# Performance work log

Measured on AMD Instinct MI355X. Metric: run time of the kernel, lower is better.

Reference implementation:

```python
import jax, jax.numpy as jnp
import numpy as np

B, N, E, H, HID = 4, 2048, 1024, 16, 4096
D = E // H
EPS = 1e-5


def setup_inputs() -> dict:
    key = jax.random.key(0)
    ks = jax.random.split(key, 8)
    s = 0.02
    return {
        "x": jax.random.normal(ks[0], (B, N, E), dtype=jnp.float32),
        "Wqkv": jax.random.normal(ks[1], (3 * E, E), dtype=jnp.float32) * s,
        "bqkv": jnp.zeros((3 * E,), dtype=jnp.float32),
        "Wo": jax.random.normal(ks[2], (E, E), dtype=jnp.float32) * s,
        "bo": jnp.zeros((E,), dtype=jnp.float32),
        "ln1_g": jnp.ones((E,), dtype=jnp.float32),
        "ln1_b": jnp.zeros((E,), dtype=jnp.float32),
        "W1": jax.random.normal(ks[3], (HID, E), dtype=jnp.float32) * s,
        "bf1": jnp.zeros((HID,), dtype=jnp.float32),
        "W2": jax.random.normal(ks[4], (E, HID), dtype=jnp.float32) * s,
        "bf2": jnp.zeros((E,), dtype=jnp.float32),
        "ln2_g": jnp.ones((E,), dtype=jnp.float32),
        "ln2_b": jnp.zeros((E,), dtype=jnp.float32),
    }


def _layernorm(x, g, b):
    m = jnp.mean(x, axis=-1, keepdims=True)
    v = jnp.mean(jnp.square(x - m), axis=-1, keepdims=True)
    return (x - m) * jax.lax.rsqrt(v + EPS) * g + b


def reference(x, Wqkv, bqkv, Wo, bo, ln1_g, ln1_b, W1, bf1, W2, bf2, ln2_g, ln2_b):
    Bx, Nx, Ex = x.shape
    # --- MultiHeadSelfAttention (faithful to original, including its einsum-label quirk) ---
    qkv = x @ Wqkv.T + bqkv                                   # (B,N,3E)
    qkv = qkv.reshape(Bx, Nx, 3, H, D).transpose(2, 0, 3, 1, 4)  # (3,B,H,N,D)
    q, k, v = qkv[0], qkv[1], qkv[2]                          # each (B,H,N,D)
    # original torch labels: q/k interpreted as (n,q,h,d) -> energy (B,N,H,H)
    energy = jnp.einsum('nqhd,nkhd->nhqk', q, k)
    attention = jax.nn.softmax(energy / (Ex ** 0.5), axis=-1)  # softmax over heads axis
    out = jnp.einsum('nhql,nlhd->nqhd', attention, v).reshape(Bx, Nx, Ex)
    attn_out = out @ Wo.T + bo
    # --- residual + LN1 ---
    h = _layernorm(x + attn_out, ln1_g, ln1_b)
    # --- FFN (dropout is identity in eval) ---
    f = jax.nn.gelu(h @ W1.T + bf1, approximate=False) @ W2.T + bf2
    # --- residual + LN2 ---
    return _layernorm(h + f, ln2_g, ln2_b)
```

## Files before the change

kernel.cpp:

```cpp
#include <hip/hip_runtime.h>
#include <hip/hip_bf16.h>
#include <math.h>

typedef __hip_bfloat16 bf16;
typedef __bf16 bf8v __attribute__((ext_vector_type(8)));
typedef float f4v __attribute__((ext_vector_type(4)));

__device__ inline void storeC(bf16* p, float v) { *p = __float2bfloat16(v); }
__device__ inline void storeC(float* p, float v) { *p = v; }

__device__ inline void gld16(const void* g, void* l) {
    __builtin_amdgcn_global_load_lds(
        (__attribute__((address_space(1))) void*)g,
        (__attribute__((address_space(3))) void*)l, 16, 0, 0);
}

__global__ __launch_bounds__(256)
void cast_f2b(const float* __restrict__ X, bf16* __restrict__ Y, long n)
{
    const long i = ((long)blockIdx.x * 256 + threadIdx.x) * 4;
    if (i + 3 < n) {
        const float4 v = *(const float4*)(X + i);
        Y[i + 0] = __float2bfloat16(v.x);
        Y[i + 1] = __float2bfloat16(v.y);
        Y[i + 2] = __float2bfloat16(v.z);
        Y[i + 3] = __float2bfloat16(v.w);
    }
}

template<int ACT, bool HASRES, typename CT, int K>
__global__ __launch_bounds__(256)
void gemm_bt(const bf16* __restrict__ A, const bf16* __restrict__ W,
             const float* __restrict__ bias, const float* __restrict__ R,
             CT* __restrict__ C, int M, int N)
{
    __shared__ __align__(16) unsigned short sA[2 * 128 * 32];
    __shared__ __align__(16) unsigned short sB[2 * 128 * 32];

    const int tid  = threadIdx.x;
    const int lane = tid & 63;
    const int wave = tid >> 6;
    const long row0 = (long)blockIdx.x * 128;
    const long col0 = (long)blockIdx.y * 128;
    const int wm = (wave >> 1) * 64;
    const int wn = (wave & 1) * 64;
    const int fr = lane & 15;
    const int fk = (lane >> 4) * 8;

    const f4v fzero = {0.f, 0.f, 0.f, 0.f};
    f4v acc[4][4];
#pragma unroll
    for (int i = 0; i < 4; ++i)
#pragma unroll
        for (int j = 0; j < 4; ++j) acc[i][j] = fzero;

    const unsigned short* gA = (const unsigned short*)A + (row0 + (tid >> 2)) * (long)K + (tid & 3) * 8;
    const unsigned short* gB = (const unsigned short*)W + (col0 + (tid >> 2)) * (long)K + (tid & 3) * 8;
    unsigned short* lA0 = &sA[wave * 512];
    unsigned short* lA1 = &sA[2048 + wave * 512];
    unsigned short* lB0 = &sB[wave * 512];
    unsigned short* lB1 = &sB[2048 + wave * 512];

    gld16(gA,                lA0);
    gld16(gA + 64 * (long)K, lA1);
    gld16(gB,                lB0);
    gld16(gB + 64 * (long)K, lB1);
    __syncthreads();

    constexpr int NI = K >> 5;
#pragma unroll 2
    for (int i = 0; i < NI; ++i) {
        if (i + 1 < NI) {
            const int kn = (i + 1) << 5;
            const int nb = ((i + 1) & 1) * 4096;
            gld16(gA + kn,                lA0 + nb);
            gld16(gA + 64 * (long)K + kn, lA1 + nb);
            gld16(gB + kn,                lB0 + nb);
            gld16(gB + 64 * (long)K + kn, lB1 + nb);
        }

        const int base = (i & 1) * 4096;
        bf8v af[4], bv[4];
#pragma unroll
        for (int t = 0; t < 4; ++t) {
            af[t] = *(const bf8v*)&sA[base + (wm + t * 16 + fr) * 32 + fk];
            bv[t] = *(const bf8v*)&sB[base + (wn + t * 16 + fr) * 32 + fk];
        }
#pragma unroll
        for (int ii = 0; ii < 4; ++ii)
#pragma unroll
            for (int jj = 0; jj < 4; ++jj)
                acc[ii][jj] = __builtin_amdgcn_mfma_f32_16x16x32_bf16(af[ii], bv[jj], acc[ii][jj], 0, 0, 0);

        __syncthreads();
    }

#pragma unroll
    for (int j = 0; j < 4; ++j) {
        const long n = col0 + wn + j * 16 + fr;
        const float bvv = bias[n];
#pragma unroll
        for (int i = 0; i < 4; ++i) {
            const long mbase = row0 + wm + i * 16 + (lane >> 4) * 4;
#pragma unroll
            for (int r = 0; r < 4; ++r) {
                float v0 = acc[i][j][r] + bvv;
                if (HASRES) v0 += R[(mbase + r) * (long)N + n];
                if (ACT == 1) v0 = 0.5f * v0 * (1.f + erff(v0 * 0.70710678118654752f));
                storeC(&C[(mbase + r) * (long)N + n], v0);
            }
        }
    }
}

__global__ __launch_bounds__(256)
void attn_kernel(const bf16* __restrict__ qkv, bf16* __restrict__ scr)
{
    __shared__ float sb[4][3392];
    const int tid = threadIdx.x;
    const int wave = tid >> 6, lane = tid & 63;
    const int m = blockIdx.x * 4 + wave;

    float* q = sb[wave];
    float* k = q + 1040;
    float* v = k + 1040;
    float* a = v + 1040;

    const bf16* rowp = qkv + (size_t)m * 3072;
    for (int i = lane; i < 1024; i += 64) {
        int hh = i >> 6, dd = i & 63;
        q[hh * 65 + dd] = __bfloat162float(rowp[i]);
        k[hh * 65 + dd] = __bfloat162float(rowp[1024 + i]);
        v[hh * 65 + dd] = __bfloat162float(rowp[2048 + i]);
    }
    __syncthreads();

    const int h1 = lane & 15, qd = lane >> 4;
    float e[4];
#pragma unroll
    for (int j = 0; j < 4; ++j) {
        const float* qr = q + h1 * 65;
        const float* kr = k + (qd * 4 + j) * 65;
        float s0 = 0.f;
        for (int d = 0; d < 64; ++d) s0 += qr[d] * kr[d];
        e[j] = s0 * 0.03125f;
    }
    float mx = fmaxf(fmaxf(e[0], e[1]), fmaxf(e[2], e[3]));
    mx = fmaxf(mx, __shfl_xor(mx, 16, 64));
    mx = fmaxf(mx, __shfl_xor(mx, 32, 64));
    float p[4], ps = 0.f;
#pragma unroll
    for (int j = 0; j < 4; ++j) { p[j] = expf(e[j] - mx); ps += p[j]; }
    ps += __shfl_xor(ps, 16, 64);
    ps += __shfl_xor(ps, 32, 64);
    const float inv = 1.f / ps;
#pragma unroll
    for (int j = 0; j < 4; ++j) a[h1 * 17 + qd * 4 + j] = p[j] * inv;
    __syncthreads();

    const int h = lane & 15, dg = lane >> 4;
    float arow[16];
#pragma unroll
    for (int l2 = 0; l2 < 16; ++l2) arow[l2] = a[h * 17 + l2];
    const int b = m >> 11, j = m & 2047;
    bf16* op = scr + (((size_t)b * 2048 + h * 128 + (j >> 4)) * 1024 + (j & 15) * 64);
    for (int t = 0; t < 16; ++t) {
        const int d = dg * 16 + t;
        float o = 0.f;
#pragma unroll
        for (int l2 = 0; l2 < 16; ++l2) o += arow[l2] * v[l2 * 65 + d];
        op[d] = __float2bfloat16(o);
    }
}

__global__ __launch_bounds__(256)
void ln_kernel(const float* __restrict__ X, const float* __restrict__ G,
               const float* __restrict__ Bt, float* __restrict__ Y32,
               bf16* __restrict__ Yb)
{
    __shared__ float rs[4], rq[4];
    const int tid = threadIdx.x;
    const long row = blockIdx.x;
    const float* xp = X + row * 1024;
    float x[4];
#pragma unroll
    for (int i = 0; i < 4; ++i) x[i] = xp[tid + 256 * i];

    float s = x[0] + x[1] + x[2] + x[3];
#pragma unroll
    for (int off = 32; off; off >>= 1) s += __shfl_down(s, off, 64);
    if ((tid & 63) == 0) rs[tid >> 6] = s;
    __syncthreads();
    const float mean = (rs[0] + rs[1] + rs[2] + rs[3]) * (1.f / 1024.f);

    float qv = 0.f;
#pragma unroll
    for (int i = 0; i < 4; ++i) { float d = x[i] - mean; qv += d * d; }
#pragma unroll
    for (int off = 32; off; off >>= 1) qv += __shfl_down(qv, off, 64);
    if ((tid & 63) == 0) rq[tid >> 6] = qv;
    __syncthreads();
    const float var = (rq[0] + rq[1] + rq[2] + rq[3]) * (1.f / 1024.f);
    const float rstd = rsqrtf(var + 1e-5f);

#pragma unroll
    for (int i = 0; i < 4; ++i) {
        const int e = tid + 256 * i;
        const float yv = (x[i] - mean) * rstd * G[e] + Bt[e];
        Y32[row * 1024 + e] = yv;
        if (Yb) Yb[row * 1024 + e] = __float2bfloat16(yv);
    }
}

extern "C" void kernel_launch(void* const* d_in, const int* in_sizes, int n_in,
                              void* d_out, int out_size, void* d_ws, size_t ws_size,
                              hipStream_t stream)
{
    (void)in_sizes; (void)n_in; (void)out_size;
    const float* x    = (const float*)d_in[0];
    const float* Wqkv = (const float*)d_in[1];
    const float* bqkv = (const float*)d_in[2];
    const float* Wo   = (const float*)d_in[3];
    const float* bo   = (const float*)d_in[4];
    const float* g1   = (const float*)d_in[5];
    const float* b1   = (const float*)d_in[6];
    const float* W1   = (const float*)d_in[7];
    const float* bf1  = (const float*)d_in[8];
    const float* W2   = (const float*)d_in[9];
    const float* bf2  = (const float*)d_in[10];
    const float* g2   = (const float*)d_in[11];
    const float* b2   = (const float*)d_in[12];
    float* out = (float*)d_out;

    if (ws_size < 125829120ULL) return;

    char* ws = (char*)d_ws;
    bf16* qkv   = (bf16*)(ws + 0);
    float* t    = (float*)(ws + 0);
    bf16* u     = (bf16*)(ws + 0);
    bf16* Wqkvb = (bf16*)(ws + 67108864);
    bf16* Wob   = (bf16*)(ws + 73400320);
    bf16* W1b   = (bf16*)(ws + 75497472);
    bf16* W2b   = (bf16*)(ws + 83886080);
    bf16* xb    = (bf16*)(ws + 92274688);
    bf16* scr   = (bf16*)(ws + 92274688);
    bf16* hb    = (bf16*)(ws + 109051904);
    float* h    = out;

    cast_f2b<<<8192, 256, 0, stream>>>(x,    xb,    8388608);
    cast_f2b<<<3072, 256, 0, stream>>>(Wqkv, Wqkvb, 3145728);
    cast_f2b<<<1024, 256, 0, stream>>>(Wo,   Wob,   1048576);
    cast_f2b<<<4096, 256, 0, stream>>>(W1,   W1b,   4194304);
    cast_f2b<<<4096, 256, 0, stream>>>(W2,   W2b,   4194304);

    gemm_bt<0, false, bf16, 1024><<<dim3(64, 24), 256, 0, stream>>>(xb, Wqkvb, bqkv, nullptr, qkv, 8192, 3072);
    attn_kernel<<<2048, 256, 0, stream>>>(qkv, scr);
    gemm_bt<0, true, float, 1024><<<dim3(64, 8), 256, 0, stream>>>(scr, Wob, bo, x, t, 8192, 1024);
    ln_kernel<<<8192, 256, 0, stream>>>(t, g1, b1, h, hb);
    gemm_bt<1, false, bf16, 1024><<<dim3(64, 32), 256, 0, stream>>>(hb, W1b, bf1, nullptr, u, 8192, 4096);
    gemm_bt<0, true, float, 4096><<<dim3(64, 8), 256, 0, stream>>>(u, W2b, bf2, h, out, 8192, 1024);
    ln_kernel<<<8192, 256, 0, stream>>>(out, g2, b2, out, nullptr);
}
```

Baseline: 514.9 us.

## Replace 128x128 GEMM with 256-row tiles, 4-stage LDS pipeline and swizzle

Replaces the 128x128 double-buffered bf16 GEMM with a 512-thread kernel that computes 256xBN tiles (BN 256 or 128). It adds a 4-slot LDS ring with explicit vmcnt waits, an XOR swizzle to avoid LDS bank conflicts, an XCD-aware block-id remap, and s_setprio around the MFMA bursts. The aim is more data reuse per block and better overlap of global loads with matrix math. In exchange it uses much more LDS (up to 128 KB dynamic) and more registers, and the grid is smaller, which may limit occupancy and cause wave quantisation on the smaller GEMMs.

```diff
diff --git a/kernel.cpp b/kernel.cpp
--- a/kernel.cpp
+++ b/kernel.cpp
@@ -28,84 +28,110 @@
     }
 }
 
-template<int ACT, bool HASRES, typename CT, int K>
-__global__ __launch_bounds__(256)
-void gemm_bt(const bf16* __restrict__ A, const bf16* __restrict__ W,
-             const float* __restrict__ bias, const float* __restrict__ R,
-             CT* __restrict__ C, int M, int N)
-{
-    __shared__ __align__(16) unsigned short sA[2 * 128 * 32];
-    __shared__ __align__(16) unsigned short sB[2 * 128 * 32];
+template<int ACT, bool HASRES, typename CT, int K, int BN>
+__global__ __launch_bounds__(512, 2)
+void gemm256(const bf16* __restrict__ A, const bf16* __restrict__ W,
+             const float* __restrict__ bias, const float* __restrict__ Rr,
+             CT* __restrict__ C, int N)
+{
+    extern __shared__ __align__(16) unsigned short lds[];
+    constexpr int NT   = K / 32;
+    constexpr int NREP = BN / 64;
+    constexpr int A_SH = 256 * 32;
+    constexpr int SLOT = A_SH + BN * 32;
+
+    int id = blockIdx.y * gridDim.x + blockIdx.x;
+    const int nwg = gridDim.x * gridDim.y;
+    id = (id & 7) * (nwg >> 3) + (id >> 3);
+    const int bm = id % gridDim.x;
+    const int bn = id / gridDim.x;
+    const long row0 = (long)bm * 256;
+    const long col0 = (long)bn * BN;
 
     const int tid  = threadIdx.x;
     const int lane = tid & 63;
     const int wave = tid >> 6;
-    const long row0 = (long)blockIdx.x * 128;
-    const long col0 = (long)blockIdx.y * 128;
-    const int wm = (wave >> 1) * 64;
-    const int wn = (wave & 1) * 64;
+    const int wm = wave >> 2;
+    const int wn = wave & 3;
     const int fr = lane & 15;
-    const int fk = (lane >> 4) * 8;
-
-    const f4v fzero = {0.f, 0.f, 0.f, 0.f};
-    f4v acc[4][4];
-#pragma unroll
-    for (int i = 0; i < 4; ++i)
-#pragma unroll
-        for (int j = 0; j < 4; ++j) acc[i][j] = fzero;
-
-    const unsigned short* gA = (const unsigned short*)A + (row0 + (tid >> 2)) * (long)K + (tid & 3) * 8;
-    const unsigned short* gB = (const unsigned short*)W + (col0 + (tid >> 2)) * (long)K + (tid & 3) * 8;
-    unsigned short* lA0 = &sA[wave * 512];
-    unsigned short* lA1 = &sA[2048 + wave * 512];
-    unsigned short* lB0 = &sB[wave * 512];
-    unsigned short* lB1 = &sB[2048 + wave * 512];
-
-    gld16(gA,                lA0);
-    gld16(gA + 64 * (long)K, lA1);
-    gld16(gB,                lB0);
-    gld16(gB + 64 * (long)K, lB1);
-    __syncthreads();
-
-    constexpr int NI = K >> 5;
-#pragma unroll 2
-    for (int i = 0; i < NI; ++i) {
-        if (i + 1 < NI) {
-            const int kn = (i + 1) << 5;
-            const int nb = ((i + 1) & 1) * 4096;
-            gld16(gA + kn,                lA0 + nb);
-            gld16(gA + 64 * (long)K + kn, lA1 + nb);
-            gld16(gB + kn,                lB0 + nb);
-            gld16(gB + 64 * (long)K + kn, lB1 + nb);
+    const int ksw = (((lane >> 4) ^ ((lane >> 2) & 3)) << 3);
+
+    const int srow = tid >> 2;
+    const int csrc = (tid & 3) ^ ((srow >> 2) & 3);
+    const unsigned short* gA = (const unsigned short*)A + (row0 + srow) * (long)K + csrc * 8;
+    const unsigned short* gB = (const unsigned short*)W + (col0 + srow) * (long)K + csrc * 8;
+    unsigned short* const wbase = lds + wave * 512;
+
+    auto stage = [&](int t) {
+        const long k0 = (long)t * 32;
+        unsigned short* sl = wbase + (t & 3) * SLOT;
+        gld16(gA + k0,                 sl);
+        gld16(gA + 128 * (long)K + k0, sl + 4096);
+        gld16(gB + k0,                 sl + A_SH);
+        if constexpr (BN == 256)
+            gld16(gB + 128 * (long)K + k0, sl + A_SH + 4096);
+    };
+
+    f4v acc[8][NREP];
+#pragma unroll
+    for (int i = 0; i < 8; ++i)
+#pragma unroll
+        for (int j = 0; j < NREP; ++j) acc[i][j] = {0.f, 0.f, 0.f, 0.f};
+
+    stage(0); stage(1); stage(2);
+
+#pragma unroll 4
+    for (int t = 0; t < NT; ++t) {
+        if constexpr (BN == 256) {
+            if (t + 2 < NT)      asm volatile("s_waitcnt vmcnt(8)" ::: "memory");
+            else if (t + 1 < NT) asm volatile("s_waitcnt vmcnt(4)" ::: "memory");
+            else                 asm volatile("s_waitcnt vmcnt(0)" ::: "memory");
+        } else {
+            if (t + 2 < NT)      asm volatile("s_waitcnt vmcnt(6)" ::: "memory");
+            else if (t + 1 < NT) asm volatile("s_waitcnt vmcnt(3)" ::: "memory");
+            else                 asm volatile("s_waitcnt vmcnt(0)" ::: "memory");
         }
-
-        const int base = (i & 1) * 4096;
-        bf8v af[4], bv[4];
-#pragma unroll
-        for (int t = 0; t < 4; ++t) {
-            af[t] = *(const bf8v*)&sA[base + (wm + t * 16 + fr) * 32 + fk];
-            bv[t] = *(const bf8v*)&sB[base + (wn + t * 16 + fr) * 32 + fk];
+        __builtin_amdgcn_s_barrier();
+        __builtin_amdgcn_sched_barrier(0);
+        if (t + 3 < NT) stage(t + 3);
+
+        const unsigned short* sA = lds + (t & 3) * SLOT;
+        const unsigned short* sB = sA + A_SH;
+
+        bf8v bfrag[NREP];
+#pragma unroll
+        for (int ni = 0; ni < NREP; ++ni)
+            bfrag[ni] = *(const bf8v*)&sB[(wn * (NREP * 16) + ni * 16 + fr) * 32 + ksw];
+
+#pragma unroll
+        for (int ph = 0; ph < 2; ++ph) {
+            bf8v afrag[4];
+#pragma unroll
+            for (int mi = 0; mi < 4; ++mi)
+                afrag[mi] = *(const bf8v*)&sA[(wm * 128 + ph * 64 + mi * 16 + fr) * 32 + ksw];
+            __builtin_amdgcn_s_setprio(1);
+#pragma unroll
+            for (int mi = 0; mi < 4; ++mi)
+#pragma unroll
+                for (int ni = 0; ni < NREP; ++ni)
+                    acc[ph * 4 + mi][ni] = __builtin_amdgcn_mfma_f32_16x16x32_bf16(
+                        afrag[mi], bfrag[ni], acc[ph * 4 + mi][ni], 0, 0, 0);
+            __builtin_amdgcn_s_setprio(0);
         }
-#pragma unroll
-        for (int ii = 0; ii < 4; ++ii)
-#pragma unroll
-            for (int jj = 0; jj < 4; ++jj)
-                acc[ii][jj] = __builtin_amdgcn_mfma_f32_16x16x32_bf16(af[ii], bv[jj], acc[ii][jj], 0, 0, 0);
-
-        __syncthreads();
-    }
-
-#pragma unroll
-    for (int j = 0; j < 4; ++j) {
-        const long n = col0 + wn + j * 16 + fr;
+    }
+    __builtin_amdgcn_sched_barrier(0);
+
+#pragma unroll
+    for (int ni = 0; ni < NREP; ++ni) {
+        const long n = col0 + wn * (NREP * 16) + ni * 16 + fr;
         const float bvv = bias[n];
 #pragma unroll
-        for (int i = 0; i < 4; ++i) {
-            const long mbase = row0 + wm + i * 16 + (lane >> 4) * 4;
+        for (int mi = 0; mi < 8; ++mi) {
+            const long mbase = row0 + wm * 128 + mi * 16 + (lane >> 4) * 4;
 #pragma unroll
             for (int r = 0; r < 4; ++r) {
-                float v0 = acc[i][j][r] + bvv;
-                if (HASRES) v0 += R[(mbase + r) * (long)N + n];
+                float v0 = acc[mi][ni][r] + bvv;
+                if (HASRES) v0 += Rr[(mbase + r) * (long)N + n];
                 if (ACT == 1) v0 = 0.5f * v0 * (1.f + erff(v0 * 0.70710678118654752f));
                 storeC(&C[(mbase + r) * (long)N + n], v0);
             }
@@ -253,11 +279,11 @@
     cast_f2b<<<4096, 256, 0, stream>>>(W1,   W1b,   4194304);
     cast_f2b<<<4096, 256, 0, stream>>>(W2,   W2b,   4194304);
 
-    gemm_bt<0, false, bf16, 1024><<<dim3(64, 24), 256, 0, stream>>>(xb, Wqkvb, bqkv, nullptr, qkv, 8192, 3072);
+    gemm256<0, false, bf16, 1024, 256><<<dim3(32, 12), 512, 131072, stream>>>(xb, Wqkvb, bqkv, nullptr, qkv, 3072);
     attn_kernel<<<2048, 256, 0, stream>>>(qkv, scr);
-    gemm_bt<0, true, float, 1024><<<dim3(64, 8), 256, 0, stream>>>(scr, Wob, bo, x, t, 8192, 1024);
+    gemm256<0, true, float, 1024, 128><<<dim3(32, 8), 512, 98304, stream>>>(scr, Wob, bo, x, t, 1024);
     ln_kernel<<<8192, 256, 0, stream>>>(t, g1, b1, h, hb);
-    gemm_bt<1, false, bf16, 1024><<<dim3(64, 32), 256, 0, stream>>>(hb, W1b, bf1, nullptr, u, 8192, 4096);
-    gemm_bt<0, true, float, 4096><<<dim3(64, 8), 256, 0, stream>>>(u, W2b, bf2, h, out, 8192, 1024);
+    gemm256<1, false, bf16, 1024, 256><<<dim3(32, 16), 512, 131072, stream>>>(hb, W1b, bf1, nullptr, u, 4096);
+    gemm256<0, true, float, 4096, 128><<<dim3(32, 8), 512, 98304, stream>>>(u, W2b, bf2, h, out, 1024);
     ln_kernel<<<8192, 256, 0, stream>>>(out, g2, b2, out, nullptr);
 }
```

New measurement: 532.9 us. +3.5%, slower.
